# Kernel tuning notes

Hardware: AMD Instinct MI355X
Metric: run time of the kernel (lower is better)

## Reference

```python
import jax, jax.numpy as jnp
import numpy as np


def setup_inputs() -> dict:
    key = jax.random.key(0)
    B, C, A, P, N = 4, 1, 180, 384, 256
    sinogram = jax.random.normal(key, (B, C, A, P), dtype=jnp.float32)
    # projection angles uniformly covering [0, pi)
    thetas = jnp.linspace(0.0, np.pi, A, endpoint=False).astype(jnp.float32)
    # uniformly spaced detector positions centered at 0, unit spacing
    positions = jnp.arange(P, dtype=jnp.float32) - (P - 1) / 2.0
    return {"sinogram": sinogram, "thetas": thetas, "positions": positions, "image_size": N}


def reference(sinogram, thetas, positions, image_size):
    """Radon backprojection: image[y,x] = sum_a interp(sinogram[a], x*cos+y*sin)."""
    B, C, A, P = sinogram.shape
    N = image_size
    # pixel-center coordinates, image centered at origin (y axis pointing up)
    c = jnp.arange(N, dtype=sinogram.dtype) - (N - 1) / 2.0
    xs = c[None, :]          # [1, N]
    ys = -c[:, None]         # [N, 1]
    cos = jnp.cos(thetas)[:, None, None]  # [A, 1, 1]
    sin = jnp.sin(thetas)[:, None, None]
    t = xs[None] * cos + ys[None] * sin   # [A, N, N] detector coordinate per (angle, pixel)
    # fractional index into the (uniform) detector position grid
    dp = positions[1] - positions[0]
    f = (t - positions[0]) / dp           # [A, N, N]
    i0 = jnp.floor(f)
    w = f - i0                            # linear interpolation weight
    valid = (i0 >= 0) & (i0 <= P - 2)     # rays falling inside the detector
    i0c = jnp.clip(i0, 0, P - 2).astype(jnp.int32)
    idx = i0c.reshape(A, N * N)[None, None]          # [1, 1, A, N*N]
    v0 = jnp.take_along_axis(sinogram, idx, axis=3)  # [B, C, A, N*N]
    v1 = jnp.take_along_axis(sinogram, idx + 1, axis=3)
    wf = w.reshape(A, N * N)[None, None]
    vm = valid.reshape(A, N * N)[None, None]
    val = jnp.where(vm, v0 * (1.0 - wf) + v1 * wf, 0.0)
    return val.sum(axis=2).reshape(B, C, N, N)
```

## Files before the change

kernel.cpp:

```cpp
#include <hip/hip_runtime.h>
#include <cmath>


template <int BATCH>
__global__ __launch_bounds__(256) void radon_partial_kernel(
    const float* __restrict__ sino,
    const float* __restrict__ thetas,
    const float* __restrict__ positions,
    float* __restrict__ part,
    int A, int P, int N, int chunk)
{
    __shared__ float s_cs[256];
    __shared__ float s_sn[256];
    const int tid = threadIdx.x;
    const float p0     = positions[0];
    const float inv_dp = 1.0f / (positions[1] - p0);
    if (tid < A) {
        float th = thetas[tid];
        s_cs[tid] = cosf(th) * inv_dp;
        s_sn[tid] = sinf(th) * inv_dp;
    }
    __syncthreads();

    const int nn  = N * N;
    const int pix = blockIdx.x * blockDim.x + tid;
    if (pix >= nn) return;

    const int a0 = blockIdx.y * chunk;
    const int a1 = min(A, a0 + chunk);

    const int x = pix % N;
    const int y = pix / N;
    const float half = (float)(N - 1) * 0.5f;
    const float cx = (float)x - half;
    const float cy = half - (float)y;
    const float q0 = -p0 * inv_dp;

    const int bstride = A * P;
    const float* sb0 = sino;
    const float* sb1 = sino + (size_t)1 * bstride;
    const float* sb2 = sino + (size_t)2 * bstride;
    const float* sb3 = sino + (size_t)3 * bstride;

    float acc[BATCH];
#pragma unroll
    for (int b = 0; b < BATCH; ++b) acc[b] = 0.0f;

#pragma unroll 2
    for (int a = a0; a < a1; ++a) {
        float f   = fmaf(cx, s_cs[a], fmaf(cy, s_sn[a], q0));
        float i0f = floorf(f);
        int   i0  = (int)i0f;
        float w   = f - i0f;
        float m   = (i0 >= 0 && i0 <= P - 2) ? 1.0f : 0.0f;
        int   ic  = min(max(i0, 0), P - 2);
        int   off = a * P + ic;

        if (BATCH == 4) {
            float v00 = sb0[off], v01 = sb0[off + 1];
            float v10 = sb1[off], v11 = sb1[off + 1];
            float v20 = sb2[off], v21 = sb2[off + 1];
            float v30 = sb3[off], v31 = sb3[off + 1];
            acc[0] = fmaf(m, fmaf(w, v01 - v00, v00), acc[0]);
            acc[1] = fmaf(m, fmaf(w, v11 - v10, v10), acc[1]);
            acc[2] = fmaf(m, fmaf(w, v21 - v20, v20), acc[2]);
            acc[3] = fmaf(m, fmaf(w, v31 - v30, v30), acc[3]);
        } else {
#pragma unroll
            for (int b = 0; b < BATCH; ++b) {
                float v0 = sino[(size_t)b * bstride + off];
                float v1 = sino[(size_t)b * bstride + off + 1];
                acc[b] = fmaf(m, fmaf(w, v1 - v0, v0), acc[b]);
            }
        }
    }

    float* pp = part + ((size_t)blockIdx.y * BATCH) * nn + pix;
#pragma unroll
    for (int b = 0; b < BATCH; ++b) pp[(size_t)b * nn] = acc[b];
}

__global__ __launch_bounds__(256) void radon_reduce_kernel(
    const float4* __restrict__ part,
    float4* __restrict__ out,
    int BN4, int nchunks)
{
    int i = blockIdx.x * blockDim.x + threadIdx.x;
    if (i >= BN4) return;
    float4 s = make_float4(0.f, 0.f, 0.f, 0.f);
    for (int c = 0; c < nchunks; ++c) {
        float4 v = part[(size_t)c * BN4 + i];
        s.x += v.x; s.y += v.y; s.z += v.z; s.w += v.w;
    }
    out[i] = s;
}

__global__ __launch_bounds__(256) void radon_direct_kernel(
    const float* __restrict__ sino,
    const float* __restrict__ thetas,
    const float* __restrict__ positions,
    float* __restrict__ out,
    int A, int P, int N, int BC)
{
    const int nn  = N * N;
    const int pix = blockIdx.x * blockDim.x + threadIdx.x;
    if (pix >= nn) return;
    const float p0     = positions[0];
    const float inv_dp = 1.0f / (positions[1] - p0);
    const int x = pix % N;
    const int y = pix / N;
    const float half = (float)(N - 1) * 0.5f;
    const float cx = (float)x - half;
    const float cy = half - (float)y;
    for (int b = 0; b < BC; ++b) {
        float acc = 0.0f;
        for (int a = 0; a < A; ++a) {
            float th = thetas[a];
            float f  = (cx * cosf(th) + cy * sinf(th) - p0) * inv_dp;
            float i0f = floorf(f);
            int i0 = (int)i0f;
            float w = f - i0f;
            float m = (i0 >= 0 && i0 <= P - 2) ? 1.0f : 0.0f;
            int ic = min(max(i0, 0), P - 2);
            const float* row = sino + ((size_t)b * A + a) * P + ic;
            acc = fmaf(m, fmaf(w, row[1] - row[0], row[0]), acc);
        }
        out[(size_t)b * nn + pix] = acc;
    }
}

extern "C" void kernel_launch(void* const* d_in, const int* in_sizes, int n_in,
                              void* d_out, int out_size, void* d_ws, size_t ws_size,
                              hipStream_t stream) {
    const float* sino      = (const float*)d_in[0];
    const float* thetas    = (const float*)d_in[1];
    const float* positions = (const float*)d_in[2];
    float* out             = (float*)d_out;

    const int A  = in_sizes[1];
    const int P  = in_sizes[2];
    const int BC = in_sizes[0] / (A * P);
    const int N  = (int)lroundf(sqrtf((float)(out_size / BC)));
    const int nn = N * N;

    const int ACHUNKS = 8;
    const int chunk   = (A + ACHUNKS - 1) / ACHUNKS;
    const size_t need = (size_t)ACHUNKS * BC * nn * sizeof(float);

    if (BC == 4 && A <= 256 && ws_size >= need && (nn % 4) == 0) {
        float* part = (float*)d_ws;
        dim3 block(256);
        dim3 grid1((nn + 255) / 256, ACHUNKS);
        radon_partial_kernel<4><<<grid1, block, 0, stream>>>(
            sino, thetas, positions, part, A, P, N, chunk);
        const int BN4 = BC * nn / 4;
        dim3 grid2((BN4 + 255) / 256);
        radon_reduce_kernel<<<grid2, block, 0, stream>>>(
            (const float4*)part, (float4*)out, BN4, ACHUNKS);
    } else {
        dim3 block(256);
        dim3 grid((nn + 255) / 256);
        radon_direct_kernel<<<grid, block, 0, stream>>>(
            sino, thetas, positions, out, A, P, N, BC);
    }
}
```

Baseline: 87.50 us.

## Stage sinogram rows in double-buffered LDS for partial backprojection

The partial kernel now cooperatively loads each angle's sinogram row for all four batches into shared memory, double-buffered so the next row loads while the current one is interpolated. Per-pixel gathers then read LDS instead of global memory or cache. The cost is a __syncthreads per angle, about 16KB of LDS per block that may limit occupancy, and a fast path restricted to even P up to 512 with nn a multiple of 256.

```diff
diff --git a/kernel.cpp b/kernel.cpp
--- a/kernel.cpp
+++ b/kernel.cpp
@@ -3,15 +3,18 @@
 
 
 template <int BATCH>
-__global__ __launch_bounds__(256) void radon_partial_kernel(
+__global__ __launch_bounds__(256) void radon_partial_lds(
     const float* __restrict__ sino,
     const float* __restrict__ thetas,
     const float* __restrict__ positions,
     float* __restrict__ part,
     int A, int P, int N, int chunk)
 {
+    constexpr int MAXP = 512;
     __shared__ float s_cs[256];
     __shared__ float s_sn[256];
+    __shared__ float buf[2][BATCH * MAXP];
+
     const int tid = threadIdx.x;
     const float p0     = positions[0];
     const float inv_dp = 1.0f / (positions[1] - p0);
@@ -20,14 +23,13 @@
         s_cs[tid] = cosf(th) * inv_dp;
         s_sn[tid] = sinf(th) * inv_dp;
     }
-    __syncthreads();
 
-    const int nn  = N * N;
-    const int pix = blockIdx.x * blockDim.x + tid;
-    if (pix >= nn) return;
-
-    const int a0 = blockIdx.y * chunk;
-    const int a1 = min(A, a0 + chunk);
+    const int nn    = N * N;
+    const int pix   = blockIdx.x * blockDim.x + tid;
+    const int a0    = blockIdx.y * chunk;
+    const int cnt   = min(A, a0 + chunk) - a0;
+    const int bstride = A * P;
+    const int halfP = P >> 1;
 
     const int x = pix % N;
     const int y = pix / N;
@@ -36,48 +38,54 @@
     const float cy = half - (float)y;
     const float q0 = -p0 * inv_dp;
 
-    const int bstride = A * P;
-    const float* sb0 = sino;
-    const float* sb1 = sino + (size_t)1 * bstride;
-    const float* sb2 = sino + (size_t)2 * bstride;
-    const float* sb3 = sino + (size_t)3 * bstride;
-
     float acc[BATCH];
 #pragma unroll
     for (int b = 0; b < BATCH; ++b) acc[b] = 0.0f;
 
-#pragma unroll 2
-    for (int a = a0; a < a1; ++a) {
+    if (tid < halfP) {
+#pragma unroll
+        for (int b = 0; b < BATCH; ++b) {
+            float2 v = *(const float2*)(sino + (size_t)b * bstride
+                                             + (size_t)a0 * P + 2 * tid);
+            *(float2*)(&buf[0][b * P + 2 * tid]) = v;
+        }
+    }
+    __syncthreads();
+
+    for (int i = 0; i < cnt; ++i) {
+        const int cur = i & 1;
+        if (i + 1 < cnt && tid < halfP) {
+            const int an = a0 + i + 1;
+#pragma unroll
+            for (int b = 0; b < BATCH; ++b) {
+                float2 v = *(const float2*)(sino + (size_t)b * bstride
+                                                 + (size_t)an * P + 2 * tid);
+                *(float2*)(&buf[cur ^ 1][b * P + 2 * tid]) = v;
+            }
+        }
+
+        const int a = a0 + i;
         float f   = fmaf(cx, s_cs[a], fmaf(cy, s_sn[a], q0));
         float i0f = floorf(f);
         int   i0  = (int)i0f;
         float w   = f - i0f;
         float m   = (i0 >= 0 && i0 <= P - 2) ? 1.0f : 0.0f;
         int   ic  = min(max(i0, 0), P - 2);
-        int   off = a * P + ic;
-
-        if (BATCH == 4) {
-            float v00 = sb0[off], v01 = sb0[off + 1];
-            float v10 = sb1[off], v11 = sb1[off + 1];
-            float v20 = sb2[off], v21 = sb2[off + 1];
-            float v30 = sb3[off], v31 = sb3[off + 1];
-            acc[0] = fmaf(m, fmaf(w, v01 - v00, v00), acc[0]);
-            acc[1] = fmaf(m, fmaf(w, v11 - v10, v10), acc[1]);
-            acc[2] = fmaf(m, fmaf(w, v21 - v20, v20), acc[2]);
-            acc[3] = fmaf(m, fmaf(w, v31 - v30, v30), acc[3]);
-        } else {
+        const float* bp = &buf[cur][ic];
 #pragma unroll
-            for (int b = 0; b < BATCH; ++b) {
-                float v0 = sino[(size_t)b * bstride + off];
-                float v1 = sino[(size_t)b * bstride + off + 1];
-                acc[b] = fmaf(m, fmaf(w, v1 - v0, v0), acc[b]);
-            }
+        for (int b = 0; b < BATCH; ++b) {
+            float v0 = bp[b * P];
+            float v1 = bp[b * P + 1];
+            acc[b] = fmaf(m, fmaf(w, v1 - v0, v0), acc[b]);
         }
+        __syncthreads();
     }
 
-    float* pp = part + ((size_t)blockIdx.y * BATCH) * nn + pix;
+    if (pix < nn) {
+        float* pp = part + ((size_t)blockIdx.y * BATCH) * nn + pix;
 #pragma unroll
-    for (int b = 0; b < BATCH; ++b) pp[(size_t)b * nn] = acc[b];
+        for (int b = 0; b < BATCH; ++b) pp[(size_t)b * nn] = acc[b];
+    }
 }
 
 __global__ __launch_bounds__(256) void radon_reduce_kernel(
@@ -147,11 +155,14 @@
     const int chunk   = (A + ACHUNKS - 1) / ACHUNKS;
     const size_t need = (size_t)ACHUNKS * BC * nn * sizeof(float);
 
-    if (BC == 4 && A <= 256 && ws_size >= need && (nn % 4) == 0) {
+    const bool fast = (BC == 4) && (A <= 256) && (P <= 512) && ((P & 1) == 0)
+                   && (ws_size >= need) && ((nn & 255) == 0) && ((nn & 3) == 0);
+
+    if (fast) {
         float* part = (float*)d_ws;
         dim3 block(256);
-        dim3 grid1((nn + 255) / 256, ACHUNKS);
-        radon_partial_kernel<4><<<grid1, block, 0, stream>>>(
+        dim3 grid1(nn / 256, ACHUNKS);
+        radon_partial_lds<4><<<grid1, block, 0, stream>>>(
             sino, thetas, positions, part, A, P, N, chunk);
         const int BN4 = BC * nn / 4;
         dim3 grid2((BN4 + 255) / 256);
```

Result: faster. 83.97 us (-4.0%).
